# Kernel tuning notes

Hardware: AMD Instinct MI355X
Metric: run time of the kernel (lower is better)

The kernel has to match this reference:

```python
import jax, jax.numpy as jnp
import numpy as np

N = 100000   # nodes
E = 1600000  # edges (avg degree 16)
D = 64       # in_dim
H = 64       # hidden_dim
NEG_SLOPE = 0.2


def setup_inputs() -> dict:
    key = jax.random.key(0)
    ks = jax.random.split(key, 10)
    s = 0.1  # param init scale
    return {
        "x": jax.random.normal(ks[0], (N, D), jnp.float32),
        "edge_index": jax.random.randint(ks[1], (2, E), 0, N, dtype=jnp.int64),
        "h": jax.random.normal(ks[2], (1, N, H), jnp.float32),
        "c": jax.random.normal(ks[3], (1, N, H), jnp.float32),
        "W_gat": jax.random.normal(ks[4], (D, H), jnp.float32) * s,
        "att_src": jax.random.normal(ks[5], (H,), jnp.float32) * s,
        "att_dst": jax.random.normal(ks[6], (H,), jnp.float32) * s,
        "bias_gat": jax.random.normal(ks[7], (H,), jnp.float32) * s,
        "W_ih": jax.random.normal(ks[8], (4 * H, H), jnp.float32) * s,
        "W_hh": jax.random.normal(ks[9], (4 * H, H), jnp.float32) * s,
    }


def reference(x, edge_index, h, c, W_gat, att_src, att_dst, bias_gat, W_ih, W_hh):
    src, dst = edge_index[0], edge_index[1]  # message j -> i

    # ---- Breadth: GATConv (heads=1) + tanh ----
    xs = x @ W_gat                             # [N, H] projected features
    a_src = xs @ att_src                       # [N]
    a_dst = xs @ att_dst                       # [N]
    e = jax.nn.leaky_relu(a_src[src] + a_dst[dst], NEG_SLOPE)  # [E]
    # scatter-softmax over incoming edges of each destination node
    m = jax.lax.stop_gradient(jax.ops.segment_max(e, dst, num_segments=N))
    p = jnp.exp(e - m[dst])
    z = jax.ops.segment_sum(p, dst, num_segments=N)
    alpha = p / (z[dst] + 1e-16)               # [E]
    agg = jax.ops.segment_sum(xs[src] * alpha[:, None], dst, num_segments=N)
    xb = jnp.tanh(agg + bias_gat)              # [N, H]

    # ---- Depth: single-step bias-free LSTM ----
    h0, c0 = h[0], c[0]                        # [N, H]
    gates = xb @ W_ih.T + h0 @ W_hh.T          # [N, 4H]
    i, f, g, o = jnp.split(gates, 4, axis=-1)  # torch gate order i,f,g,o
    c1 = jax.nn.sigmoid(f) * c0 + jax.nn.sigmoid(i) * jnp.tanh(g)
    h1 = jax.nn.sigmoid(o) * jnp.tanh(c1)
    return h1, h1[None], c1[None]
```

## Files before the change

kernel.cpp:

```cpp
#include <hip/hip_runtime.h>
#include <cmath>

#define NN 100000
#define EE 1600000
#define NB 1563
#define CAP 1344
#define EPB 25
#define NTILE 6250
#define PROJB 1563
#define CVTB 3125

using bf16x8 = __attribute__((ext_vector_type(8))) __bf16;
using f32x4  = __attribute__((ext_vector_type(4))) float;

__device__ __forceinline__ unsigned short f2bf(float f) {
  __bf16 b = (__bf16)f;
  return __builtin_bit_cast(unsigned short, b);
}
__device__ __forceinline__ float bflo(unsigned int u) {
  return __uint_as_float(u << 16);
}
__device__ __forceinline__ float bfhi(unsigned int u) {
  return __uint_as_float(u & 0xffff0000u);
}
__device__ __forceinline__ float sigmoidf_(float v) {
  return 1.0f / (1.0f + __expf(-v));
}
__device__ __forceinline__ float tanhfast(float v) {
  return 1.0f - 2.0f / (1.0f + __expf(2.0f * v));
}
__device__ __forceinline__ bf16x8 cvt8(float4 a, float4 b) {
  bf16x8 r;
  r[0]=(__bf16)a.x; r[1]=(__bf16)a.y; r[2]=(__bf16)a.z; r[3]=(__bf16)a.w;
  r[4]=(__bf16)b.x; r[5]=(__bf16)b.y; r[6]=(__bf16)b.z; r[7]=(__bf16)b.w;
  return r;
}

__global__ __launch_bounds__(128) void k_prep(
    const float* __restrict__ Wih, const float* __restrict__ Whh,
    const float* __restrict__ Wg,
    unsigned short* __restrict__ wperm, unsigned short* __restrict__ wgp)
{
  if (blockIdx.x < 256) {
    const int p = blockIdx.x, k = threadIdx.x;
    const int g = p & 3;
    const int h = (p >> 4) + ((p >> 2) & 3) * 16;
    const int row = g*64 + h;
    const float v = (k < 64) ? Wih[row*64 + k] : Whh[row*64 + (k - 64)];
    const int gp = (k >> 3) ^ (p & 15);
    wperm[p*128 + gp*8 + (k & 7)] = f2bf(v);
  } else {
    for (int idx = threadIdx.x; idx < 4096; idx += 128) {
      const int lane = idx >> 6, r = idx & 63;
      const int nt = r >> 4, kf = (r >> 3) & 1, j = r & 7;
      const int m = lane & 15, quad = lane >> 4;
      wgp[idx] = f2bf(Wg[(kf*32 + quad*8 + j)*64 + nt*16 + m]);
    }
  }
}

__global__ __launch_bounds__(256) void k_binproj(
    const int* __restrict__ ei, int* __restrict__ bcursor,
    unsigned int* __restrict__ binned,
    const float* __restrict__ x, const unsigned short* __restrict__ wgp,
    const float* __restrict__ att_s, const float* __restrict__ att_d,
    unsigned short* __restrict__ xs16, float* __restrict__ a_src,
    float* __restrict__ a_dst,
    const float* __restrict__ h0, unsigned short* __restrict__ h16)
{
  if (blockIdx.x < 256) {
    __shared__ int cnt[NB];
    __shared__ int gbase[NB];
    const int tid = threadIdx.x;
    const size_t base = (size_t)blockIdx.x * 256 * EPB;

    for (int b = tid; b < NB; b += 256) cnt[b] = 0;
    __syncthreads();

    unsigned int pay[EPB];
    int bidx[EPB], pos[EPB];
    #pragma unroll
    for (int j = 0; j < EPB; ++j) {
      const size_t e = base + (size_t)j*256 + tid;
      if (e < EE) {
        const int s = ei[e];
        const int d = ei[EE + e];
        bidx[j] = d >> 6;
        pay[j] = (unsigned)s | ((unsigned)(d & 63) << 17);
        pos[j] = atomicAdd(&cnt[bidx[j]], 1);
      } else {
        bidx[j] = -1;
      }
    }
    __syncthreads();

    for (int b = tid; b < NB; b += 256) {
      const int c = cnt[b];
      gbase[b] = c ? atomicAdd(&bcursor[b*16], c) : 0;
    }
    __syncthreads();

    #pragma unroll
    for (int j = 0; j < EPB; ++j) {
      if (bidx[j] >= 0) {
        const int g = gbase[bidx[j]] + pos[j];
        if (g < CAP) binned[(size_t)bidx[j]*CAP + g] = pay[j];
      }
    }
  } else if (blockIdx.x < 256 + PROJB) {
    const int lane = threadIdx.x & 63;
    const int wave = threadIdx.x >> 6;
    const int tile = (blockIdx.x - 256) * 4 + wave;
    if (tile >= NTILE) return;
    const int m = lane & 15, quad = lane >> 4;

    bf16x8 bfrag[4][2];
    {
      const unsigned short* wp = wgp + lane*64;
      #pragma unroll
      for (int nt = 0; nt < 4; ++nt)
        #pragma unroll
        for (int kf = 0; kf < 2; ++kf)
          bfrag[nt][kf] = *(const bf16x8*)(wp + nt*16 + kf*8);
    }

    const int row = tile*16 + m;
    bf16x8 afrag[2];
    #pragma unroll
    for (int kf = 0; kf < 2; ++kf) {
      const float4* p = (const float4*)(x + (size_t)row*64 + kf*32 + quad*8);
      afrag[kf] = cvt8(p[0], p[1]);
    }

    f32x4 acc[4];
    #pragma unroll
    for (int nt = 0; nt < 4; ++nt) acc[nt] = f32x4{0.f, 0.f, 0.f, 0.f};
    #pragma unroll
    for (int nt = 0; nt < 4; ++nt)
      #pragma unroll
      for (int kf = 0; kf < 2; ++kf)
        acc[nt] = __builtin_amdgcn_mfma_f32_16x16x32_bf16(
            afrag[kf], bfrag[nt][kf], acc[nt], 0, 0, 0);

    float ss[4] = {0.f,0.f,0.f,0.f}, sd[4] = {0.f,0.f,0.f,0.f};
    #pragma unroll
    for (int nt = 0; nt < 4; ++nt) {
      const float av = att_s[nt*16 + m], dv = att_d[nt*16 + m];
      #pragma unroll
      for (int r = 0; r < 4; ++r) {
        const float v = acc[nt][r];
        xs16[(size_t)(tile*16 + quad*4 + r)*64 + nt*16 + m] = f2bf(v);
        ss[r] += v * av;
        sd[r] += v * dv;
      }
    }
    #pragma unroll
    for (int off = 1; off < 16; off <<= 1) {
      #pragma unroll
      for (int r = 0; r < 4; ++r) {
        ss[r] += __shfl_xor(ss[r], off);
        sd[r] += __shfl_xor(sd[r], off);
      }
    }
    if (m == 0) {
      #pragma unroll
      for (int r = 0; r < 4; ++r) {
        a_src[tile*16 + quad*4 + r] = ss[r];
        a_dst[tile*16 + quad*4 + r] = sd[r];
      }
    }
  } else {
    const int idx = (blockIdx.x - 256 - PROJB)*256 + threadIdx.x;
    const float* p = h0 + (size_t)idx*8;
    const bf16x8 v = cvt8(*(const float4*)p, *(const float4*)(p + 4));
    *(bf16x8*)(h16 + (size_t)idx*8) = v;
  }
}

__global__ __launch_bounds__(256) void k_agg(
    const int* __restrict__ bcursor, const unsigned int* __restrict__ binned,
    const float* __restrict__ a_src, const float* __restrict__ a_dst,
    const unsigned short* __restrict__ xs16, const float* __restrict__ bias,
    unsigned short* __restrict__ xb16)
{
  __shared__ uint2 raw2[CAP];
  __shared__ uint2 csre[CAP];
  __shared__ float zsum[64], invzsh[64], adsh[64];
  __shared__ int cnt[64], offs[64], cursor[64];
  const int b = blockIdx.x;
  const int tid = threadIdx.x;
  const int ne = min(bcursor[b*16], CAP);

  if (tid < 64) {
    cnt[tid] = 0;
    zsum[tid] = 0.f;
    const int node = b*64 + tid;
    adsh[tid] = (node < NN) ? a_dst[node] : 0.f;
  }
  __syncthreads();

  for (int i = tid; i < ne; i += 256) {
    const unsigned int w = binned[(size_t)b*CAP + i];
    const int s = (int)(w & 0x1FFFFu);
    const int dl = (int)((w >> 17) & 63u);
    float ev = a_src[s] + adsh[dl];
    ev = (ev >= 0.f) ? ev : 0.2f*ev;
    const float pv = __expf(ev);
    raw2[i] = make_uint2(w, __float_as_uint(pv));
    atomicAdd(&cnt[dl], 1);
    atomicAdd(&zsum[dl], pv);
  }
  __syncthreads();

  if (tid < 64) {
    const int v = cnt[tid];
    int inc = v;
    #pragma unroll
    for (int dd = 1; dd < 64; dd <<= 1) {
      const int o = __shfl_up(inc, dd, 64);
      if (tid >= dd) inc += o;
    }
    offs[tid] = inc - v;
    cursor[tid] = inc - v;
    invzsh[tid] = 1.f / (zsum[tid] + 1e-16f);
  }
  __syncthreads();

  for (int i = tid; i < ne; i += 256) {
    const uint2 r = raw2[i];
    const int dl = (int)((r.x >> 17) & 63u);
    const int pos = atomicAdd(&cursor[dl], 1);
    csre[pos] = make_uint2(r.x & 0x1FFFFu, r.y);
  }
  __syncthreads();

  const int lane = tid & 63;
  const int wv = tid >> 6;
  const int grp = lane >> 4, l16 = lane & 15;
  const float4 b4 = *(const float4*)(bias + l16*4);
  const unsigned short* xrow = xs16 + l16*4;
  for (int t = 0; t < 16; ++t) {
    const int nl = wv*16 + t;
    const int node = b*64 + nl;
    if (node >= NN) break;
    const int bse = offs[nl];
    const int dg = cnt[nl];
    float acc0=0.f, acc1=0.f, acc2=0.f, acc3=0.f;
    for (int e = grp; e < dg; e += 4) {
      const uint2 sp = csre[bse + e];
      const float pv = __uint_as_float(sp.y);
      const uint2 rw = *(const uint2*)(xrow + (size_t)sp.x*64);
      acc0 += pv*bflo(rw.x); acc1 += pv*bfhi(rw.x);
      acc2 += pv*bflo(rw.y); acc3 += pv*bfhi(rw.y);
    }
    #pragma unroll
    for (int off = 16; off < 64; off <<= 1) {
      acc0 += __shfl_xor(acc0, off);
      acc1 += __shfl_xor(acc1, off);
      acc2 += __shfl_xor(acc2, off);
      acc3 += __shfl_xor(acc3, off);
    }
    if (lane < 16) {
      const float invz = invzsh[nl];
      ushort4 o;
      o.x = f2bf(tanhfast(acc0*invz + b4.x));
      o.y = f2bf(tanhfast(acc1*invz + b4.y));
      o.z = f2bf(tanhfast(acc2*invz + b4.z));
      o.w = f2bf(tanhfast(acc3*invz + b4.w));
      *(ushort4*)(xb16 + (size_t)node*64 + l16*4) = o;
    }
  }
}

__global__ __launch_bounds__(1024, 2) void k_lstm(
    const unsigned short* __restrict__ xb16, const unsigned short* __restrict__ h16,
    const float* __restrict__ c0, const unsigned short* __restrict__ wperm,
    float* __restrict__ out)
{
  __shared__ unsigned short wlds[256*128];
  const int tid = threadIdx.x;
  {
    const float4* gs = (const float4*)wperm;
    float4* ls = (float4*)wlds;
    #pragma unroll
    for (int i = 0; i < 4; ++i) ls[tid + i*1024] = gs[tid + i*1024];
  }
  __syncthreads();

  const int w = tid >> 6, lane = tid & 63;
  const int wv = w & 3, tsub = w >> 2;
  const int m = lane & 15, quad = lane >> 4;
  const int tile = blockIdx.x*4 + tsub;
  if (tile >= NTILE) return;
  const int node = tile*16 + m;

  bf16x8 bfr[4];
  bfr[0] = *(const bf16x8*)(xb16 + (size_t)node*64 + quad*8);
  bfr[1] = *(const bf16x8*)(xb16 + (size_t)node*64 + 32 + quad*8);
  bfr[2] = *(const bf16x8*)(h16 + (size_t)node*64 + quad*8);
  bfr[3] = *(const bf16x8*)(h16 + (size_t)node*64 + 32 + quad*8);

  const int q32 = (m >> 2) & 3;
  const int base = (wv*64 + m)*256 + ((quad ^ (m & 3)) << 4);
  const char* lb = (const char*)wlds;
  const int a0 = base + ((0 ^ q32) << 6);
  const int a1 = base + ((1 ^ q32) << 6);
  const int a2 = base + ((2 ^ q32) << 6);
  const int a3 = base + ((3 ^ q32) << 6);

  f32x4 acc[4];
  #pragma unroll
  for (int u = 0; u < 4; ++u) acc[u] = f32x4{0.f, 0.f, 0.f, 0.f};
  #pragma unroll
  for (int u = 0; u < 4; ++u) {
    const int uo = u*4096;
    const bf16x8 w0 = *(const bf16x8*)(lb + a0 + uo);
    const bf16x8 w1 = *(const bf16x8*)(lb + a1 + uo);
    const bf16x8 w2 = *(const bf16x8*)(lb + a2 + uo);
    const bf16x8 w3 = *(const bf16x8*)(lb + a3 + uo);
    acc[u] = __builtin_amdgcn_mfma_f32_16x16x32_bf16(w0, bfr[0], acc[u], 0, 0, 0);
    acc[u] = __builtin_amdgcn_mfma_f32_16x16x32_bf16(w1, bfr[1], acc[u], 0, 0, 0);
    acc[u] = __builtin_amdgcn_mfma_f32_16x16x32_bf16(w2, bfr[2], acc[u], 0, 0, 0);
    acc[u] = __builtin_amdgcn_mfma_f32_16x16x32_bf16(w3, bfr[3], acc[u], 0, 0, 0);
  }

  const size_t obase = (size_t)node*64 + quad*16 + wv*4;
  const float4 cv = *(const float4*)(c0 + obase);
  const float cvv[4] = {cv.x, cv.y, cv.z, cv.w};
  float h1a[4], c1a[4];
  #pragma unroll
  for (int u = 0; u < 4; ++u) {
    const float gi = acc[u][0], gf = acc[u][1];
    const float gg = acc[u][2], go = acc[u][3];
    const float c1 = sigmoidf_(gf)*cvv[u] + sigmoidf_(gi)*tanhfast(gg);
    h1a[u] = sigmoidf_(go)*tanhfast(c1);
    c1a[u] = c1;
  }
  const float4 hv  = make_float4(h1a[0], h1a[1], h1a[2], h1a[3]);
  const float4 c1v = make_float4(c1a[0], c1a[1], c1a[2], c1a[3]);
  *(float4*)(out + obase) = hv;
  *(float4*)(out + (size_t)NN*64 + obase) = hv;
  *(float4*)(out + (size_t)2*NN*64 + obase) = c1v;
}

extern "C" void kernel_launch(void* const* d_in, const int* in_sizes, int n_in,
                              void* d_out, int out_size, void* d_ws, size_t ws_size,
                              hipStream_t stream) {
  const float* x    = (const float*)d_in[0];
  const int*   ei   = (const int*)d_in[1];
  const float* h    = (const float*)d_in[2];
  const float* c    = (const float*)d_in[3];
  const float* Wg   = (const float*)d_in[4];
  const float* atts = (const float*)d_in[5];
  const float* attd = (const float*)d_in[6];
  const float* bg   = (const float*)d_in[7];
  const float* Wih  = (const float*)d_in[8];
  const float* Whh  = (const float*)d_in[9];
  float* out = (float*)d_out;

  char* w = (char*)d_ws;
  unsigned short* xs16  = (unsigned short*)w; w += (size_t)NN*64*2;
  unsigned short* xb16  = (unsigned short*)w; w += (size_t)NN*64*2;
  unsigned short* h16   = (unsigned short*)w; w += (size_t)NN*64*2;
  unsigned short* wperm = (unsigned short*)w; w += (size_t)256*128*2;
  unsigned short* wgp   = (unsigned short*)w; w += (size_t)4096*2;
  unsigned int*   binned= (unsigned int*)w;  w += (size_t)NB*CAP*4;
  float* a_src = (float*)w; w += (size_t)NN*4;
  float* a_dst = (float*)w; w += (size_t)NN*4;
  int* bcursor = (int*)w;   w += (size_t)NB*16*4;

  hipMemsetAsync(bcursor, 0, (size_t)NB*16*4, stream);

  k_prep    <<<257, 128, 0, stream>>>(Wih, Whh, Wg, wperm, wgp);
  k_binproj <<<256 + PROJB + CVTB, 256, 0, stream>>>(
      ei, bcursor, binned, x, wgp, atts, attd, xs16, a_src, a_dst, h, h16);
  k_agg     <<<NB, 256, 0, stream>>>(bcursor, binned, a_src, a_dst, xs16, bg, xb16);
  k_lstm    <<<PROJB, 1024, 0, stream>>>(xb16, h16, c, wperm, out);
}
```

Before: 289.4 us.

## Keep edge data in registers, prefetch CSR entries, and persist LSTM blocks

In k_agg, the edge words and exp values now stay in per-thread registers across six unrolled slots instead of going through an LDS staging array. The a_src gathers are batched ahead of use, and the next CSR entry is prefetched inside the aggregation loop. k_lstm becomes a grid-stride persistent kernel with 512 blocks, so the 64KB weight load into LDS is paid once per block rather than once per tile group. Costs are higher register pressure, and correctness depends on ne never exceeding 6*256=1536; since CAP is 1344, that holds.

```diff
diff --git a/kernel.cpp b/kernel.cpp
--- a/kernel.cpp
+++ b/kernel.cpp
@@ -183,8 +183,7 @@
     const unsigned short* __restrict__ xs16, const float* __restrict__ bias,
     unsigned short* __restrict__ xb16)
 {
-  __shared__ uint2 raw2[CAP];
-  __shared__ uint2 csre[CAP];
+  __shared__ uint2 csre[CAP + 8];
   __shared__ float zsum[64], invzsh[64], adsh[64];
   __shared__ int cnt[64], offs[64], cursor[64];
   const int b = blockIdx.x;
@@ -199,16 +198,33 @@
   }
   __syncthreads();
 
-  for (int i = tid; i < ne; i += 256) {
-    const unsigned int w = binned[(size_t)b*CAP + i];
-    const int s = (int)(w & 0x1FFFFu);
-    const int dl = (int)((w >> 17) & 63u);
-    float ev = a_src[s] + adsh[dl];
-    ev = (ev >= 0.f) ? ev : 0.2f*ev;
-    const float pv = __expf(ev);
-    raw2[i] = make_uint2(w, __float_as_uint(pv));
-    atomicAdd(&cnt[dl], 1);
-    atomicAdd(&zsum[dl], pv);
+  unsigned int w6[6];
+  float pv6[6];
+  {
+    float as6[6];
+    #pragma unroll
+    for (int k = 0; k < 6; ++k) {
+      const int i = tid + k*256;
+      w6[k] = (i < ne) ? binned[(size_t)b*CAP + i] : 0u;
+    }
+    #pragma unroll
+    for (int k = 0; k < 6; ++k) {
+      const int i = tid + k*256;
+      as6[k] = (i < ne) ? a_src[w6[k] & 0x1FFFFu] : 0.f;
+    }
+    #pragma unroll
+    for (int k = 0; k < 6; ++k) {
+      const int i = tid + k*256;
+      if (i < ne) {
+        const int dl = (int)((w6[k] >> 17) & 63u);
+        float ev = as6[k] + adsh[dl];
+        ev = (ev >= 0.f) ? ev : 0.2f*ev;
+        const float pv = __expf(ev);
+        pv6[k] = pv;
+        atomicAdd(&cnt[dl], 1);
+        atomicAdd(&zsum[dl], pv);
+      }
+    }
   }
   __syncthreads();
 
@@ -226,11 +242,15 @@
   }
   __syncthreads();
 
-  for (int i = tid; i < ne; i += 256) {
-    const uint2 r = raw2[i];
-    const int dl = (int)((r.x >> 17) & 63u);
-    const int pos = atomicAdd(&cursor[dl], 1);
-    csre[pos] = make_uint2(r.x & 0x1FFFFu, r.y);
+  #pragma unroll
+  for (int k = 0; k < 6; ++k) {
+    const int i = tid + k*256;
+    if (i < ne) {
+      const unsigned int w = w6[k];
+      const int dl = (int)((w >> 17) & 63u);
+      const int pos = atomicAdd(&cursor[dl], 1);
+      csre[pos] = make_uint2(w & 0x1FFFFu, __float_as_uint(pv6[k]));
+    }
   }
   __syncthreads();
 
@@ -246,12 +266,14 @@
     const int bse = offs[nl];
     const int dg = cnt[nl];
     float acc0=0.f, acc1=0.f, acc2=0.f, acc3=0.f;
+    uint2 sp = csre[bse + grp];
     for (int e = grp; e < dg; e += 4) {
-      const uint2 sp = csre[bse + e];
+      const uint2 spn = csre[bse + e + 4];
       const float pv = __uint_as_float(sp.y);
       const uint2 rw = *(const uint2*)(xrow + (size_t)sp.x*64);
       acc0 += pv*bflo(rw.x); acc1 += pv*bfhi(rw.x);
       acc2 += pv*bflo(rw.y); acc3 += pv*bfhi(rw.y);
+      sp = spn;
     }
     #pragma unroll
     for (int off = 16; off < 64; off <<= 1) {
@@ -290,15 +312,6 @@
   const int w = tid >> 6, lane = tid & 63;
   const int wv = w & 3, tsub = w >> 2;
   const int m = lane & 15, quad = lane >> 4;
-  const int tile = blockIdx.x*4 + tsub;
-  if (tile >= NTILE) return;
-  const int node = tile*16 + m;
-
-  bf16x8 bfr[4];
-  bfr[0] = *(const bf16x8*)(xb16 + (size_t)node*64 + quad*8);
-  bfr[1] = *(const bf16x8*)(xb16 + (size_t)node*64 + 32 + quad*8);
-  bfr[2] = *(const bf16x8*)(h16 + (size_t)node*64 + quad*8);
-  bfr[3] = *(const bf16x8*)(h16 + (size_t)node*64 + 32 + quad*8);
 
   const int q32 = (m >> 2) & 3;
   const int base = (wv*64 + m)*256 + ((quad ^ (m & 3)) << 4);
@@ -308,39 +321,51 @@
   const int a2 = base + ((2 ^ q32) << 6);
   const int a3 = base + ((3 ^ q32) << 6);
 
-  f32x4 acc[4];
-  #pragma unroll
-  for (int u = 0; u < 4; ++u) acc[u] = f32x4{0.f, 0.f, 0.f, 0.f};
-  #pragma unroll
-  for (int u = 0; u < 4; ++u) {
-    const int uo = u*4096;
-    const bf16x8 w0 = *(const bf16x8*)(lb + a0 + uo);
-    const bf16x8 w1 = *(const bf16x8*)(lb + a1 + uo);
-    const bf16x8 w2 = *(const bf16x8*)(lb + a2 + uo);
-    const bf16x8 w3 = *(const bf16x8*)(lb + a3 + uo);
-    acc[u] = __builtin_amdgcn_mfma_f32_16x16x32_bf16(w0, bfr[0], acc[u], 0, 0, 0);
-    acc[u] = __builtin_amdgcn_mfma_f32_16x16x32_bf16(w1, bfr[1], acc[u], 0, 0, 0);
-    acc[u] = __builtin_amdgcn_mfma_f32_16x16x32_bf16(w2, bfr[2], acc[u], 0, 0, 0);
-    acc[u] = __builtin_amdgcn_mfma_f32_16x16x32_bf16(w3, bfr[3], acc[u], 0, 0, 0);
-  }
-
-  const size_t obase = (size_t)node*64 + quad*16 + wv*4;
-  const float4 cv = *(const float4*)(c0 + obase);
-  const float cvv[4] = {cv.x, cv.y, cv.z, cv.w};
-  float h1a[4], c1a[4];
-  #pragma unroll
-  for (int u = 0; u < 4; ++u) {
-    const float gi = acc[u][0], gf = acc[u][1];
-    const float gg = acc[u][2], go = acc[u][3];
-    const float c1 = sigmoidf_(gf)*cvv[u] + sigmoidf_(gi)*tanhfast(gg);
-    h1a[u] = sigmoidf_(go)*tanhfast(c1);
-    c1a[u] = c1;
-  }
-  const float4 hv  = make_float4(h1a[0], h1a[1], h1a[2], h1a[3]);
-  const float4 c1v = make_float4(c1a[0], c1a[1], c1a[2], c1a[3]);
-  *(float4*)(out + obase) = hv;
-  *(float4*)(out + (size_t)NN*64 + obase) = hv;
-  *(float4*)(out + (size_t)2*NN*64 + obase) = c1v;
+  for (int tg = blockIdx.x; tg < PROJB; tg += gridDim.x) {
+    const int tile = tg*4 + tsub;
+    if (tile >= NTILE) continue;
+    const int node = tile*16 + m;
+
+    bf16x8 bfr[4];
+    bfr[0] = *(const bf16x8*)(xb16 + (size_t)node*64 + quad*8);
+    bfr[1] = *(const bf16x8*)(xb16 + (size_t)node*64 + 32 + quad*8);
+    bfr[2] = *(const bf16x8*)(h16 + (size_t)node*64 + quad*8);
+    bfr[3] = *(const bf16x8*)(h16 + (size_t)node*64 + 32 + quad*8);
+
+    f32x4 acc[4];
+    #pragma unroll
+    for (int u = 0; u < 4; ++u) acc[u] = f32x4{0.f, 0.f, 0.f, 0.f};
+    #pragma unroll
+    for (int u = 0; u < 4; ++u) {
+      const int uo = u*4096;
+      const bf16x8 w0 = *(const bf16x8*)(lb + a0 + uo);
+      const bf16x8 w1 = *(const bf16x8*)(lb + a1 + uo);
+      const bf16x8 w2 = *(const bf16x8*)(lb + a2 + uo);
+      const bf16x8 w3 = *(const bf16x8*)(lb + a3 + uo);
+      acc[u] = __builtin_amdgcn_mfma_f32_16x16x32_bf16(w0, bfr[0], acc[u], 0, 0, 0);
+      acc[u] = __builtin_amdgcn_mfma_f32_16x16x32_bf16(w1, bfr[1], acc[u], 0, 0, 0);
+      acc[u] = __builtin_amdgcn_mfma_f32_16x16x32_bf16(w2, bfr[2], acc[u], 0, 0, 0);
+      acc[u] = __builtin_amdgcn_mfma_f32_16x16x32_bf16(w3, bfr[3], acc[u], 0, 0, 0);
+    }
+
+    const size_t obase = (size_t)node*64 + quad*16 + wv*4;
+    const float4 cv = *(const float4*)(c0 + obase);
+    const float cvv[4] = {cv.x, cv.y, cv.z, cv.w};
+    float h1a[4], c1a[4];
+    #pragma unroll
+    for (int u = 0; u < 4; ++u) {
+      const float gi = acc[u][0], gf = acc[u][1];
+      const float gg = acc[u][2], go = acc[u][3];
+      const float c1 = sigmoidf_(gf)*cvv[u] + sigmoidf_(gi)*tanhfast(gg);
+      h1a[u] = sigmoidf_(go)*tanhfast(c1);
+      c1a[u] = c1;
+    }
+    const float4 hv  = make_float4(h1a[0], h1a[1], h1a[2], h1a[3]);
+    const float4 c1v = make_float4(c1a[0], c1a[1], c1a[2], c1a[3]);
+    *(float4*)(out + obase) = hv;
+    *(float4*)(out + (size_t)NN*64 + obase) = hv;
+    *(float4*)(out + (size_t)2*NN*64 + obase) = c1v;
+  }
 }
 
 extern "C" void kernel_launch(void* const* d_in, const int* in_sizes, int n_in,
@@ -375,5 +400,5 @@
   k_binproj <<<256 + PROJB + CVTB, 256, 0, stream>>>(
       ei, bcursor, binned, x, wgp, atts, attd, xs16, a_src, a_dst, h, h16);
   k_agg     <<<NB, 256, 0, stream>>>(bcursor, binned, a_src, a_dst, xs16, bg, xb16);
-  k_lstm    <<<PROJB, 1024, 0, stream>>>(xb16, h16, c, wperm, out);
-}
+  k_lstm    <<<512, 1024, 0, stream>>>(xb16, h16, c, wperm, out);
+}
```

After: 293.8 us. Within noise of the previous version (+1.5%).
